# Kernel tuning notes

Hardware: AMD Instinct MI355X
Metric: run time of the kernel (lower is better)

Reference implementation:

```python
import jax, jax.numpy as jnp
import numpy as np

NUM_HEADS = 16
HEAD_DIM = 64


def setup_inputs() -> dict:
    key = jax.random.key(0)
    k1, k2, k3 = jax.random.split(key, 3)
    dim = NUM_HEADS * HEAD_DIM  # 1024
    x = jax.random.normal(k1, (1, 4096, dim), dtype=jnp.float32)
    w_qkv = jax.random.normal(k2, (dim, 3 * dim), dtype=jnp.float32) * (dim ** -0.5)
    w_out = jax.random.normal(k3, (dim, dim), dtype=jnp.float32) * (dim ** -0.5)
    b_out = jnp.zeros((dim,), dtype=jnp.float32)
    return {"x": x, "w_qkv": w_qkv, "w_out": w_out, "b_out": b_out}


def reference(x, w_qkv, w_out, b_out):
    b, n, dim = x.shape
    h, d = NUM_HEADS, HEAD_DIM
    qkv = x @ w_qkv                                  # [b, n, 3*h*d]
    q, k, v = jnp.split(qkv, 3, axis=-1)
    q = q.reshape(b, n, h, d)
    k = k.reshape(b, n, h, d)
    v = v.reshape(b, n, h, d)  # NOTE: unused below — source module's bug uses K as V
    q = q * (d ** -0.5)
    # The chunked online-softmax in the source is mathematically exact softmax
    # attention; express it directly. Scores layout matches einsum '...qhd,...khd->...qhk'.
    scores = jnp.einsum('bqhd,bkhd->bqhk', q, k)     # [b, n, h, n]
    attn = jax.nn.softmax(scores, axis=-1)
    # Faithful to source bug: value_chunk was sliced from `key`, so V := K here.
    att = jnp.einsum('bqhk,bkhd->bqhd', attn, k)     # [b, n, h, d]
    out = att.reshape(b, n, h * d)
    return out @ w_out + b_out
```

## Files before the change

### kernel.cpp

```cpp
#include <hip/hip_runtime.h>
#include <hip/hip_bf16.h>

#define NT 4096
#define DIM 1024
#define NH 16
#define HD 64

typedef __attribute__((ext_vector_type(8))) short bf16x8;
typedef __attribute__((ext_vector_type(4))) float f32x4;
typedef __attribute__((ext_vector_type(16))) float f32x16;

__device__ __forceinline__ unsigned short f2b(float f) {
  union { float f; unsigned u; } v; v.f = f;
  unsigned r = v.u + 0x7fffu + ((v.u >> 16) & 1u);
  return (unsigned short)(r >> 16);
}
__device__ __forceinline__ float b2f(unsigned short u) {
  union { unsigned u; float f; } v; v.u = ((unsigned)u) << 16; return v.f;
}

__device__ __forceinline__ float fexp2(float x) {
#if __has_builtin(__builtin_amdgcn_exp2f)
  return __builtin_amdgcn_exp2f(x);
#else
  return exp2f(x);
#endif
}

__global__ void k_cvt(const float4* __restrict__ src, ushort4* __restrict__ dst, int n4) {
  int i = blockIdx.x * blockDim.x + threadIdx.x;
  if (i >= n4) return;
  float4 v = src[i];
  ushort4 o;
  o.x = f2b(v.x); o.y = f2b(v.y); o.z = f2b(v.z); o.w = f2b(v.w);
  dst[i] = o;
}

__global__ __launch_bounds__(256) void k_trans_w(const float* __restrict__ src, int S,
                                                 unsigned short* __restrict__ dst, int Kdim) {
  __shared__ float tile[32][33];
  int j0 = blockIdx.x * 32, k0 = blockIdx.y * 32;
  int t = threadIdx.x;
  int c = t & 31, rq = t >> 5;
#pragma unroll
  for (int i = 0; i < 4; i++) {
    int r = rq + i * 8;
    tile[r][c] = src[(size_t)(k0 + r) * S + j0 + c];
  }
  __syncthreads();
#pragma unroll
  for (int i = 0; i < 4; i++) {
    int jr = rq + i * 8;
    dst[(size_t)(j0 + jr) * Kdim + k0 + c] = f2b(tile[c][jr]);
  }
}

template <int EPI>
__global__ __launch_bounds__(256) void k_gemm(const unsigned short* __restrict__ A,
                                              const unsigned short* __restrict__ Bt,
                                              unsigned short* __restrict__ qh,
                                              unsigned short* __restrict__ krm,
                                              float* __restrict__ cout,
                                              const float* __restrict__ bias) {
  __shared__ __align__(16) unsigned short As[4096];
  __shared__ __align__(16) unsigned short Bs[4096];
  const int K = 1024;
  int m0 = blockIdx.y * 128, n0 = blockIdx.x * 128;
  int t = threadIdx.x;
  int w = t >> 6, l = t & 63;
  int wr = w >> 1, wc = w & 1;
  int lq = l & 15, lg = l >> 4;
  char* AsB = (char*)As;
  char* BsB = (char*)Bs;
  f32x4 zero = {0.f, 0.f, 0.f, 0.f};
  f32x4 acc[4][4];
#pragma unroll
  for (int i = 0; i < 4; i++)
#pragma unroll
    for (int j = 0; j < 4; j++) acc[i][j] = zero;

  for (int k0 = 0; k0 < K; k0 += 32) {
#pragma unroll
    for (int s = 0; s < 2; s++) {
      int slot = s * 256 + t;
      int row = slot >> 2;
      int cc = (slot & 3) ^ ((row >> 1) & 3);
      int db = (s * 256 + (t & 192)) * 16;
      const unsigned short* ga = A + (size_t)(m0 + row) * K + k0 + cc * 8;
      const unsigned short* gb = Bt + (size_t)(n0 + row) * K + k0 + cc * 8;
      __builtin_amdgcn_global_load_lds(
          (const __attribute__((address_space(1))) unsigned int*)ga,
          (__attribute__((address_space(3))) unsigned int*)(AsB + db), 16, 0, 0);
      __builtin_amdgcn_global_load_lds(
          (const __attribute__((address_space(1))) unsigned int*)gb,
          (__attribute__((address_space(3))) unsigned int*)(BsB + db), 16, 0, 0);
    }
    __syncthreads();
    bf16x8 af[4], bf[4];
#pragma unroll
    for (int mi = 0; mi < 4; mi++) {
      int row = wr * 64 + mi * 16 + lq;
      af[mi] = *reinterpret_cast<bf16x8*>(AsB + row * 64 + ((lg ^ ((row >> 1) & 3)) * 16));
    }
#pragma unroll
    for (int ni = 0; ni < 4; ni++) {
      int row = wc * 64 + ni * 16 + lq;
      bf[ni] = *reinterpret_cast<bf16x8*>(BsB + row * 64 + ((lg ^ ((row >> 1) & 3)) * 16));
    }
#pragma unroll
    for (int mi = 0; mi < 4; mi++)
#pragma unroll
      for (int ni = 0; ni < 4; ni++)
        acc[mi][ni] =
            __builtin_amdgcn_mfma_f32_16x16x32_bf16(af[mi], bf[ni], acc[mi][ni], 0, 0, 0);
    __syncthreads();
  }
#pragma unroll
  for (int mi = 0; mi < 4; mi++) {
#pragma unroll
    for (int ni = 0; ni < 4; ni++) {
      int j = n0 + wc * 64 + ni * 16 + lq;
#pragma unroll
      for (int r = 0; r < 4; r++) {
        int row = m0 + wr * 64 + mi * 16 + lg * 4 + r;
        float v = acc[mi][ni][r];
        if (EPI == 0) {
          if (j < DIM) {
            qh[((size_t)(j >> 6) << 18) + (size_t)row * HD + (j & 63)] =
                f2b(v * 0.18033688011112042f);
          } else {
            int jj = j - DIM;
            krm[((size_t)(jj >> 6) << 18) + (size_t)row * HD + (jj & 63)] = f2b(v);
          }
        } else {
          cout[(size_t)row * DIM + j] = v + bias[j];
        }
      }
    }
  }
}

__global__ __launch_bounds__(256) void k_transK(const unsigned short* __restrict__ krm,
                                                unsigned short* __restrict__ kt) {
  __shared__ unsigned short tile[64][72];
  int h = blockIdx.y, n0 = blockIdx.x * 64;
  int t = threadIdx.x;
  const unsigned short* src = krm + (size_t)h * NT * HD;
#pragma unroll
  for (int s = 0; s < 2; s++) {
    int slot = t + s * 256;
    int r = slot >> 3, c8 = (slot & 7) * 8;
    *reinterpret_cast<bf16x8*>(&tile[r][c8]) =
        *reinterpret_cast<const bf16x8*>(src + (size_t)(n0 + r) * HD + c8);
  }
  __syncthreads();
  unsigned short* dst = kt + (size_t)h * HD * NT;
#pragma unroll
  for (int s = 0; s < 2; s++) {
    int slot = t + s * 256;
    int dd = slot & 63, c8 = (slot >> 6) * 8;
    bf16x8 vv;
#pragma unroll
    for (int i = 0; i < 8; i++) vv[i] = (short)tile[c8 + i][dd];
    *reinterpret_cast<bf16x8*>(dst + (size_t)dd * NT + n0 + c8) = vv;
  }
}

__global__ __launch_bounds__(256, 4) void k_attn(const unsigned short* __restrict__ qh,
                                                 const unsigned short* __restrict__ krm,
                                                 const unsigned short* __restrict__ kt,
                                                 unsigned short* __restrict__ part0,
                                                 unsigned short* __restrict__ part1,
                                                 float* __restrict__ stats) {
  __shared__ __align__(16) unsigned char sbuf[2][16384];

  int hw = blockIdx.x;
  int xcd = hw & 7, idx = hw >> 3;
  int h = xcd * 2 + (idx >> 6);
  int sub = idx & 63;
  int q0 = (sub & 31) * 128;
  int kvs = sub >> 5;
  int kv_base = kvs * (NT / 2);

  unsigned short* ob = kvs ? part1 : part0;
  float* lb = stats + (size_t)kvs * (NH * NT);

  int t = threadIdx.x, w = t >> 6, l = t & 63;
  int lq = l & 31, hi = l >> 5;
  const unsigned char* Kb = (const unsigned char*)(krm + (size_t)h * NT * HD);
  const unsigned char* Tb = (const unsigned char*)(kt + (size_t)h * HD * NT);
  const unsigned short* Qb = qh + (size_t)h * NT * HD;

  int qrow = q0 + w * 32 + lq;
  bf16x8 qf[4];
#pragma unroll
  for (int ds = 0; ds < 4; ds++)
    qf[ds] = *reinterpret_cast<const bf16x8*>(Qb + (size_t)qrow * HD + ds * 16 + hi * 8);

  bf16x8 ones;
#pragma unroll
  for (int i = 0; i < 8; i++) ones[i] = (short)0x3F80;

  int rdbase = lq * 16 + hi * 1024;

  f32x16 o0, o1, lacc;
#pragma unroll
  for (int r = 0; r < 16; r++) { o0[r] = 0.f; o1[r] = 0.f; lacc[r] = 0.f; }

  auto STAGE = [&](int b, int kv0) {
    unsigned char* base = &sbuf[b][0];
#pragma unroll
    for (int i = 0; i < 4; i++) {
      int c = w * 4 + i;
      const unsigned char* g;
      if (c < 8) {
        g = Kb + (size_t)(kv0 + l) * 128 + (c >> 1) * 32 + (c & 1) * 16;
      } else {
        g = Tb + (size_t)l * 8192 + (size_t)kv0 * 2 + (c - 8) * 16;
      }
      __builtin_amdgcn_global_load_lds(
          (const __attribute__((address_space(1))) unsigned int*)g,
          (__attribute__((address_space(3))) unsigned int*)(base + c * 1024), 16, 0, 0);
    }
  };

  STAGE(0, kv_base);
  __syncthreads();

  for (int tile = 0; tile < 32; tile++) {
    int cur = tile & 1;
    if (tile < 31) STAGE(cur ^ 1, kv_base + (tile + 1) * 64);
    const unsigned char* KaB = &sbuf[cur][0];

    f32x16 s0, s1;
#pragma unroll
    for (int r = 0; r < 16; r++) { s0[r] = 0.f; s1[r] = 0.f; }
#pragma unroll
    for (int ds = 0; ds < 4; ds++) {
      bf16x8 a0 = *reinterpret_cast<const bf16x8*>(KaB + rdbase + ds * 2048);
      bf16x8 a1 = *reinterpret_cast<const bf16x8*>(KaB + rdbase + ds * 2048 + 512);
      s0 = __builtin_amdgcn_mfma_f32_32x32x16_bf16(a0, qf[ds], s0, 0, 0, 0);
      s1 = __builtin_amdgcn_mfma_f32_32x32x16_bf16(a1, qf[ds], s1, 0, 0, 0);
    }

#pragma unroll
    for (int r = 0; r < 16; r++) s0[r] = fexp2(s0[r]);
#pragma unroll
    for (int r = 0; r < 16; r++) s1[r] = fexp2(s1[r]);

    unsigned pk0[8], pk1[8];
#pragma unroll
    for (int i = 0; i < 8; i++) {
      asm("v_cvt_pk_bf16_f32 %0, %1, %2" : "=v"(pk0[i]) : "v"(s0[2 * i]), "v"(s0[2 * i + 1]));
      asm("v_cvt_pk_bf16_f32 %0, %1, %2" : "=v"(pk1[i]) : "v"(s1[2 * i]), "v"(s1[2 * i + 1]));
    }
    bf16x8 pf[4];
#pragma unroll
    for (int kb = 0; kb < 4; kb++) {
      const unsigned* pk = (kb < 2) ? pk0 : pk1;
      int m = kb & 1;
      unsigned d0 = pk[4 * m + 0], d1 = pk[4 * m + 1];
      unsigned e0 = pk[4 * m + 2], e1 = pk[4 * m + 3];
      asm volatile("v_permlane32_swap_b32 %0, %1" : "+v"(d0), "+v"(e0));
      asm volatile("v_permlane32_swap_b32 %0, %1" : "+v"(d1), "+v"(e1));
      union { unsigned u[4]; bf16x8 v; } uu;
      uu.u[0] = d0; uu.u[1] = d1; uu.u[2] = e0; uu.u[3] = e1;
      pf[kb] = uu.v;
    }

#pragma unroll
    for (int kb = 0; kb < 4; kb++) {
      bf16x8 v0 = *reinterpret_cast<const bf16x8*>(KaB + rdbase + 8192 + kb * 2048);
      o0 = __builtin_amdgcn_mfma_f32_32x32x16_bf16(pf[kb], v0, o0, 0, 0, 0);
    }
#pragma unroll
    for (int kb = 0; kb < 4; kb++) {
      bf16x8 v1 = *reinterpret_cast<const bf16x8*>(KaB + rdbase + 8192 + kb * 2048 + 512);
      o1 = __builtin_amdgcn_mfma_f32_32x32x16_bf16(pf[kb], v1, o1, 0, 0, 0);
    }
#pragma unroll
    for (int kb = 0; kb < 4; kb++)
      lacc = __builtin_amdgcn_mfma_f32_32x32x16_bf16(pf[kb], ones, lacc, 0, 0, 0);
    __syncthreads();
  }

#pragma unroll
  for (int r = 0; r < 16; r++) {
    int qr = (r & 3) + 8 * (r >> 2) + 4 * hi;
    size_t grow = (size_t)(q0 + w * 32 + qr);
    ob[grow * DIM + h * HD + lq] = f2b(o0[r]);
    ob[grow * DIM + h * HD + 32 + lq] = f2b(o1[r]);
  }
#pragma unroll
  for (int r = 0; r < 16; r++) {
    int qr = (r & 3) + 8 * (r >> 2) + 4 * hi;
    if (lq == qr) {
      lb[h * NT + q0 + w * 32 + qr] = lacc[r];
    }
  }
}

__global__ __launch_bounds__(256) void k_combine(unsigned short* __restrict__ p0b,
                                                 const unsigned short* __restrict__ p1b,
                                                 const float* __restrict__ stats) {
  int i = blockIdx.x * 256 + threadIdx.x;
  int base = i * 8;
  int q = base >> 10;
  int c = base & 1023;
  int h = c >> 6;
  float ll0 = stats[h * NT + q];
  float ll1 = stats[NH * NT + h * NT + q];
  float a = 1.0f / (ll0 + ll1);
  bf16x8 v0 = *reinterpret_cast<const bf16x8*>(p0b + base);
  bf16x8 v1 = *reinterpret_cast<const bf16x8*>(p1b + base);
  bf16x8 o;
#pragma unroll
  for (int j = 0; j < 8; j++)
    o[j] = (short)f2b((b2f((unsigned short)v0[j]) + b2f((unsigned short)v1[j])) * a);
  *reinterpret_cast<bf16x8*>(p0b + base) = o;
}

extern "C" void kernel_launch(void* const* d_in, const int* in_sizes, int n_in,
                              void* d_out, int out_size, void* d_ws, size_t ws_size,
                              hipStream_t stream) {
  const float* x = (const float*)d_in[0];
  const float* w_qkv = (const float*)d_in[1];
  const float* w_out = (const float*)d_in[2];
  const float* b_out = (const float*)d_in[3];
  float* out = (float*)d_out;

  char* ws = (char*)d_ws;
  unsigned short* xb   = (unsigned short*)(ws);
  unsigned short* wqkT = (unsigned short*)(ws + 8388608);
  unsigned short* woT  = (unsigned short*)(ws + 12582912);
  unsigned short* qhb  = (unsigned short*)(ws + 14680064);
  unsigned short* krm  = (unsigned short*)(ws + 23068672);
  unsigned short* ktb  = (unsigned short*)(ws + 31457280);
  unsigned short* attb = (unsigned short*)(ws + 39845888);
  float* stats = (float*)wqkT;

  k_cvt<<<(NT * DIM / 4 + 255) / 256, 256, 0, stream>>>((const float4*)x, (ushort4*)xb,
                                                        NT * DIM / 4);
  dim3 g1(2048 / 32, 1024 / 32);
  k_trans_w<<<g1, 256, 0, stream>>>(w_qkv, 3 * DIM, wqkT, DIM);
  dim3 g2(1024 / 32, 1024 / 32);
  k_trans_w<<<g2, 256, 0, stream>>>(w_out, DIM, woT, DIM);
  dim3 g3(2048 / 128, NT / 128);
  k_gemm<0><<<g3, 256, 0, stream>>>(xb, wqkT, qhb, krm, nullptr, nullptr);
  dim3 g4(NT / 64, NH);
  k_transK<<<g4, 256, 0, stream>>>(krm, ktb);
  k_attn<<<(NT / 128) * NH * 2, 256, 0, stream>>>(qhb, krm, ktb, attb, xb, stats);
  k_combine<<<NT * DIM / 8 / 256, 256, 0, stream>>>(attb, xb, stats);
  dim3 g5(DIM / 128, NT / 128);
  k_gemm<1><<<g5, 256, 0, stream>>>(attb, woT, nullptr, nullptr, out, b_out);
}
```

Before: 159.0 us.

## Fuse split-KV combine into output GEMM and compute softmax row sums on VALU

The separate combine kernel is removed. The output projection GEMM now loads both partial attention outputs, adds them, scales by the reciprocal of the summed row statistics, and writes the bf16 result into LDS at the swizzled position. This avoids a full read and write pass over the attention buffer and one kernel launch, but the A operand now goes through registers instead of the asynchronous global-to-LDS path, which can expose load latency in the GEMM. In the attention kernel, the extra MFMA against a vector of ones that accumulated row sums is replaced by a VALU sum of the exponentials plus a cross-half shuffle.

```diff
diff --git a/kernel.cpp b/kernel.cpp
--- a/kernel.cpp
+++ b/kernel.cpp
@@ -61,7 +61,9 @@
                                               unsigned short* __restrict__ qh,
                                               unsigned short* __restrict__ krm,
                                               float* __restrict__ cout,
-                                              const float* __restrict__ bias) {
+                                              const float* __restrict__ bias,
+                                              const unsigned short* __restrict__ A2,
+                                              const float* __restrict__ lst) {
   __shared__ __align__(16) unsigned short As[4096];
   __shared__ __align__(16) unsigned short Bs[4096];
   const int K = 1024;
@@ -86,14 +88,26 @@
       int row = slot >> 2;
       int cc = (slot & 3) ^ ((row >> 1) & 3);
       int db = (s * 256 + (t & 192)) * 16;
-      const unsigned short* ga = A + (size_t)(m0 + row) * K + k0 + cc * 8;
       const unsigned short* gb = Bt + (size_t)(n0 + row) * K + k0 + cc * 8;
-      __builtin_amdgcn_global_load_lds(
-          (const __attribute__((address_space(1))) unsigned int*)ga,
-          (__attribute__((address_space(3))) unsigned int*)(AsB + db), 16, 0, 0);
       __builtin_amdgcn_global_load_lds(
           (const __attribute__((address_space(1))) unsigned int*)gb,
           (__attribute__((address_space(3))) unsigned int*)(BsB + db), 16, 0, 0);
+      if (EPI == 0) {
+        const unsigned short* ga = A + (size_t)(m0 + row) * K + k0 + cc * 8;
+        __builtin_amdgcn_global_load_lds(
+            (const __attribute__((address_space(1))) unsigned int*)ga,
+            (__attribute__((address_space(3))) unsigned int*)(AsB + db), 16, 0, 0);
+      } else {
+        bf16x8 u0 = *reinterpret_cast<const bf16x8*>(A + (size_t)(m0 + row) * K + k0 + cc * 8);
+        bf16x8 u1 = *reinterpret_cast<const bf16x8*>(A2 + (size_t)(m0 + row) * K + k0 + cc * 8);
+        int head = k0 >> 6;
+        float ls = 1.0f / (lst[head * NT + m0 + row] + lst[NH * NT + head * NT + m0 + row]);
+        bf16x8 sm;
+#pragma unroll
+        for (int j = 0; j < 8; j++)
+          sm[j] = (short)f2b((b2f((unsigned short)u0[j]) + b2f((unsigned short)u1[j])) * ls);
+        *reinterpret_cast<bf16x8*>(AsB + row * 64 + (slot & 3) * 16) = sm;
+      }
     }
     __syncthreads();
     bf16x8 af[4], bf[4];
@@ -197,15 +211,12 @@
   for (int ds = 0; ds < 4; ds++)
     qf[ds] = *reinterpret_cast<const bf16x8*>(Qb + (size_t)qrow * HD + ds * 16 + hi * 8);
 
-  bf16x8 ones;
-#pragma unroll
-  for (int i = 0; i < 8; i++) ones[i] = (short)0x3F80;
-
   int rdbase = lq * 16 + hi * 1024;
 
-  f32x16 o0, o1, lacc;
-#pragma unroll
-  for (int r = 0; r < 16; r++) { o0[r] = 0.f; o1[r] = 0.f; lacc[r] = 0.f; }
+  f32x16 o0, o1;
+#pragma unroll
+  for (int r = 0; r < 16; r++) { o0[r] = 0.f; o1[r] = 0.f; }
+  float l_run = 0.f;
 
   auto STAGE = [&](int b, int kv0) {
     unsigned char* base = &sbuf[b][0];
@@ -248,6 +259,16 @@
 #pragma unroll
     for (int r = 0; r < 16; r++) s1[r] = fexp2(s1[r]);
 
+    float suA = 0.f, suB = 0.f, suC = 0.f, suD = 0.f;
+#pragma unroll
+    for (int r = 0; r < 16; r += 4) {
+      suA += s0[r]; suB += s0[r + 1]; suC += s0[r + 2]; suD += s0[r + 3];
+      suA += s1[r]; suB += s1[r + 1]; suC += s1[r + 2]; suD += s1[r + 3];
+    }
+    float ps = (suA + suB) + (suC + suD);
+    ps += __shfl_xor(ps, 32);
+    l_run += ps;
+
     unsigned pk0[8], pk1[8];
 #pragma unroll
     for (int i = 0; i < 8; i++) {
@@ -278,9 +299,6 @@
       bf16x8 v1 = *reinterpret_cast<const bf16x8*>(KaB + rdbase + 8192 + kb * 2048 + 512);
       o1 = __builtin_amdgcn_mfma_f32_32x32x16_bf16(pf[kb], v1, o1, 0, 0, 0);
     }
-#pragma unroll
-    for (int kb = 0; kb < 4; kb++)
-      lacc = __builtin_amdgcn_mfma_f32_32x32x16_bf16(pf[kb], ones, lacc, 0, 0, 0);
     __syncthreads();
   }
 
@@ -291,33 +309,9 @@
     ob[grow * DIM + h * HD + lq] = f2b(o0[r]);
     ob[grow * DIM + h * HD + 32 + lq] = f2b(o1[r]);
   }
-#pragma unroll
-  for (int r = 0; r < 16; r++) {
-    int qr = (r & 3) + 8 * (r >> 2) + 4 * hi;
-    if (lq == qr) {
-      lb[h * NT + q0 + w * 32 + qr] = lacc[r];
-    }
-  }
-}
-
-__global__ __launch_bounds__(256) void k_combine(unsigned short* __restrict__ p0b,
-                                                 const unsigned short* __restrict__ p1b,
-                                                 const float* __restrict__ stats) {
-  int i = blockIdx.x * 256 + threadIdx.x;
-  int base = i * 8;
-  int q = base >> 10;
-  int c = base & 1023;
-  int h = c >> 6;
-  float ll0 = stats[h * NT + q];
-  float ll1 = stats[NH * NT + h * NT + q];
-  float a = 1.0f / (ll0 + ll1);
-  bf16x8 v0 = *reinterpret_cast<const bf16x8*>(p0b + base);
-  bf16x8 v1 = *reinterpret_cast<const bf16x8*>(p1b + base);
-  bf16x8 o;
-#pragma unroll
-  for (int j = 0; j < 8; j++)
-    o[j] = (short)f2b((b2f((unsigned short)v0[j]) + b2f((unsigned short)v1[j])) * a);
-  *reinterpret_cast<bf16x8*>(p0b + base) = o;
+  if (l < 32) {
+    lb[h * NT + q0 + w * 32 + lq] = l_run;
+  }
 }
 
 extern "C" void kernel_launch(void* const* d_in, const int* in_sizes, int n_in,
@@ -346,11 +340,10 @@
   dim3 g2(1024 / 32, 1024 / 32);
   k_trans_w<<<g2, 256, 0, stream>>>(w_out, DIM, woT, DIM);
   dim3 g3(2048 / 128, NT / 128);
-  k_gemm<0><<<g3, 256, 0, stream>>>(xb, wqkT, qhb, krm, nullptr, nullptr);
+  k_gemm<0><<<g3, 256, 0, stream>>>(xb, wqkT, qhb, krm, nullptr, nullptr, nullptr, nullptr);
   dim3 g4(NT / 64, NH);
   k_transK<<<g4, 256, 0, stream>>>(krm, ktb);
   k_attn<<<(NT / 128) * NH * 2, 256, 0, stream>>>(qhb, krm, ktb, attb, xb, stats);
-  k_combine<<<NT * DIM / 8 / 256, 256, 0, stream>>>(attb, xb, stats);
   dim3 g5(DIM / 128, NT / 128);
-  k_gemm<1><<<g5, 256, 0, stream>>>(attb, woT, nullptr, nullptr, out, b_out);
-}
+  k_gemm<1><<<g5, 256, 0, stream>>>(attb, woT, nullptr, nullptr, out, b_out, xb, stats);
+}
```

Result: slower. 173.0 us (+8.8%).
